# Optimization experiments

Hardware: AMD Instinct MI355X
Metric: run time of the kernel (lower is better)

The kernel has to match this reference:

```python
import jax, jax.numpy as jnp
import numpy as np

MAX_DEG = 10
MIN_DEG = 0
N_FEAT = 128
NB_FILTER = 128
BATCH = 128
DEG_COUNT = 30000                      # atoms per degree bucket (static)
N_ATOMS = (MAX_DEG + 1) * DEG_COUNT    # 330000, atoms sorted by degree (deg0 first)
NB_AFFINE = 3 * MAX_DEG + (2 - MIN_DEG)  # 32
EPS = 1e-5


def setup_inputs() -> dict:
    key = jax.random.key(0)
    ks = jax.random.split(key, 16)
    atoms = jax.random.normal(ks[0], (N_ATOMS, N_FEAT), dtype=jnp.float32)
    membership = jax.random.randint(ks[1], (N_ATOMS,), 0, BATCH)
    # deg_slice[d] = [start, count] for degree d (atoms sorted by degree)
    deg_slice = jnp.stack([jnp.arange(MAX_DEG + 1) * DEG_COUNT,
                           jnp.full((MAX_DEG + 1,), DEG_COUNT)], axis=1)
    inp = {"atoms": atoms, "deg_slice": deg_slice, "membership": membership}
    for d in range(1, MAX_DEG + 1):
        inp[f"adj{d}"] = jax.random.randint(ks[1 + d], (DEG_COUNT, d), 0, N_ATOMS)
    glorot = (2.0 / (N_FEAT + NB_FILTER)) ** 0.5
    inp["W"] = jax.random.normal(ks[12], (NB_AFFINE, N_FEAT, NB_FILTER), dtype=jnp.float32) * glorot
    inp["b"] = jnp.zeros((NB_AFFINE, NB_FILTER), dtype=jnp.float32)
    inp["gamma"] = jnp.ones((NB_FILTER,), dtype=jnp.float32)
    inp["beta"] = jnp.zeros((NB_FILTER,), dtype=jnp.float32)
    return inp


def _self_slice(atoms, deg):
    return jax.lax.dynamic_slice_in_dim(atoms, deg * DEG_COUNT, DEG_COUNT, axis=0)


def _norm(x, gamma, beta):
    m = jnp.mean(x, axis=-1, keepdims=True)
    std = jnp.sqrt(jnp.var(x, axis=-1, keepdims=True) + EPS)
    return gamma * ((x - m) / (std + EPS)) + beta


def _forward(atoms, W, b, gamma, beta, membership, adjs):
    # W consumption order matches the TF iterator: for deg=1..max_deg -> (rel, self),
    # then deg0 self at index 2*MAX_DEG, then gather affines deg1..max_deg, deg0 last.
    rel_outs = [None] * (MAX_DEG + 1)
    gather_outs = [None] * (MAX_DEG + 1)
    for d in range(1, MAX_DEG + 1):
        neigh = jnp.sum(atoms[adjs[d - 1]], axis=1)          # (COUNT, F) gather+sum
        self_a = _self_slice(atoms, d)                        # (COUNT, F)
        i_rel, i_self = 2 * (d - 1), 2 * d - 1
        rel_outs[d] = (neigh @ W[i_rel] + b[i_rel]) + (self_a @ W[i_self] + b[i_self])
        i_g = 2 * MAX_DEG + d
        gather_outs[d] = self_a @ W[i_g] + b[i_g]
    self0 = _self_slice(atoms, 0)
    rel_outs[0] = self0 @ W[2 * MAX_DEG] + b[2 * MAX_DEG]
    gather_outs[0] = self0 @ W[NB_AFFINE - 1] + b[NB_AFFINE - 1]

    activated = jnp.concatenate(rel_outs, axis=0)             # (N_ATOMS, NB_FILTER)
    gathered = jnp.concatenate(gather_outs, axis=0)           # (N_ATOMS, NB_FILTER)
    # graph_gather: per-molecule sum (dynamic_partition + reduce_sum)
    atom_gather = jax.ops.segment_sum(gathered, membership, num_segments=BATCH)

    xn = _norm(activated, gamma, beta)                        # per-row "BN" as in source
    yn = _norm(atom_gather, gamma, beta)
    # gather_node: per-molecule max of normalized atom features
    g = jax.ops.segment_max(xn, membership, num_segments=BATCH)
    return xn, yn, g


def reference(atoms, deg_slice, membership, adj1, adj2, adj3, adj4, adj5,
              adj6, adj7, adj8, adj9, adj10, W, b, gamma, beta):
    adjs = (adj1, adj2, adj3, adj4, adj5, adj6, adj7, adj8, adj9, adj10)
    return _forward(atoms, W, b, gamma, beta, membership, adjs)
```

## Files before the change

### kernel.cpp

```cpp
#include <hip/hip_runtime.h>
#include <stdint.h>

#define MAX_DEG   10
#define DEG_COUNT 30000
#define N_ATOMS   330000
#define NF        128
#define BATCH     128
#define SORT_BLOCKS 256

typedef __attribute__((ext_vector_type(8))) short bf16x8;
typedef __attribute__((ext_vector_type(4))) float f32x4;

__device__ __forceinline__ float bf2f(unsigned short h) {
  union { unsigned u; float f; } v; v.u = ((unsigned)h) << 16; return v.f;
}
__device__ __forceinline__ unsigned short f2bf(float f) {
  union { float f; unsigned u; } v; v.f = f;
  unsigned u = v.u;
  unsigned r = (u + 0x7fffu + ((u >> 16) & 1u)) >> 16;
  return (unsigned short)r;
}

struct AdjPtrs { const int* p[10]; };

#define NEG_INF_BITS 0xFF800000

__global__ __launch_bounds__(256) void k_cast(const float4* __restrict__ src,
                                              ushort4* __restrict__ dst) {
  size_t i = (size_t)blockIdx.x * 256 + threadIdx.x;
  float4 v = src[i];
  ushort4 o;
  o.x = f2bf(v.x); o.y = f2bf(v.y); o.z = f2bf(v.z); o.w = f2bf(v.w);
  dst[i] = o;
}

__global__ __launch_bounds__(256) void k_build_b(const float* __restrict__ W,
                                                 unsigned short* __restrict__ BcatT) {
  int idx = blockIdx.x * 256 + threadIdx.x;
  if (idx >= 11 * 256 * 256) return;
  int d = idx >> 16;
  int rem = idx & 65535;
  int n = rem >> 8;
  int k = rem & 255;
  float v = 0.f;
  if (k < 128) {
    if (n < 128 && d >= 1) v = W[(2 * (d - 1)) * 16384 + k * 128 + n];
  } else {
    int ks = k - 128;
    if (n < 128) { int wi = (d >= 1) ? (2 * d - 1) : 20; v = W[wi * 16384 + ks * 128 + n]; }
    else         { int wi = (d >= 1) ? (20 + d)   : 31; v = W[wi * 16384 + ks * 128 + (n - 128)]; }
  }
  BcatT[idx] = f2bf(v);
}

__global__ __launch_bounds__(256) void k_build_bias(const float* __restrict__ b,
                                                    float* __restrict__ biascat) {
  int idx = blockIdx.x * 256 + threadIdx.x;
  if (idx >= 11 * 256) return;
  int d = idx >> 8, n = idx & 255;
  float f;
  if (n < 128) {
    if (d >= 1) f = b[(2 * (d - 1)) * 128 + n] + b[(2 * d - 1) * 128 + n];
    else        f = b[20 * 128 + n];
  } else {
    int j = n - 128;
    f = (d >= 1) ? b[(20 + d) * 128 + j] : b[31 * 128 + j];
  }
  biascat[idx] = f;
}

template<int D>
__device__ __forceinline__ void nsum_phase0(const unsigned* __restrict__ atomsU,
                                            const int* __restrict__ abase,
                                            unsigned* __restrict__ NS,
                                            int rowTile, int wave, int lane) {
  for (int it = 0; it < 16; ++it) {
    int iloc = wave * 32 + it * 2;
    int r0 = rowTile * 256 + iloc;
    int sw0 = lane ^ ((iloc & 7) << 2);
    int sw1 = lane ^ (((iloc + 1) & 7) << 2);
    if (r0 < DEG_COUNT - 1) {
      const int* a = abase + (size_t)r0 * D;
      int myIdx = (lane < 2 * D) ? a[lane] : 0;
      unsigned xs[2 * D];
#pragma unroll
      for (int j = 0; j < 2 * D; ++j) {
        int nbr = __shfl(myIdx, j, 64);
        xs[j] = atomsU[(size_t)nbr * 64 + lane];
      }
      float s0a = 0.f, s1a = 0.f, s0b = 0.f, s1b = 0.f;
#pragma unroll
      for (int j = 0; j < D; ++j) {
        s0a += bf2f((unsigned short)(xs[j] & 0xffff));
        s1a += bf2f((unsigned short)(xs[j] >> 16));
      }
#pragma unroll
      for (int j = D; j < 2 * D; ++j) {
        s0b += bf2f((unsigned short)(xs[j] & 0xffff));
        s1b += bf2f((unsigned short)(xs[j] >> 16));
      }
      NS[(size_t)iloc * 64 + sw0]       = (unsigned)f2bf(s0a) | ((unsigned)f2bf(s1a) << 16);
      NS[(size_t)(iloc + 1) * 64 + sw1] = (unsigned)f2bf(s0b) | ((unsigned)f2bf(s1b) << 16);
    } else {
      const int* a = abase + (size_t)(DEG_COUNT - 1) * D;
      int myIdx = (lane < D) ? a[lane] : 0;
      unsigned xs[D];
#pragma unroll
      for (int j = 0; j < D; ++j) {
        int nbr = __shfl(myIdx, j, 64);
        xs[j] = atomsU[(size_t)nbr * 64 + lane];
      }
      float s0 = 0.f, s1 = 0.f;
#pragma unroll
      for (int j = 0; j < D; ++j) {
        s0 += bf2f((unsigned short)(xs[j] & 0xffff));
        s1 += bf2f((unsigned short)(xs[j] >> 16));
      }
      unsigned p = (unsigned)f2bf(s0) | ((unsigned)f2bf(s1) << 16);
      NS[(size_t)iloc * 64 + sw0] = p;
      NS[(size_t)(iloc + 1) * 64 + sw1] = p;
    }
  }
}

__global__ __launch_bounds__(512, 2) void k_gemm(
    const unsigned short* __restrict__ atomsBf,
    AdjPtrs adj,
    const unsigned short* __restrict__ BcatT,
    const float* __restrict__ biascat,
    const float* __restrict__ gamma,
    const float* __restrict__ beta,
    float* __restrict__ out0,
    unsigned short* __restrict__ gath)
{
  const int d = blockIdx.y;
  const int rowTile = blockIdx.x;
  const int tid = threadIdx.x;
  const int lane = tid & 63;
  const int wave = tid >> 6;
  const int m16 = lane & 15;
  const int g = lane >> 4;

  __shared__ unsigned short Bs[256 * 256];
  unsigned* NS = (unsigned*)Bs;

  const unsigned short* Bd = BcatT + d * 65536;
  const unsigned* atomsU = (const unsigned*)atomsBf;

  const int rowBase0 = rowTile * 256 + wave * 32;
  bf16x8 af0[8], af1[8];
  {
    int rbL = rowBase0 + m16; if (rbL > DEG_COUNT - 1) rbL = DEG_COUNT - 1;
    size_t gr = (size_t)d * DEG_COUNT + rbL;
#pragma unroll
    for (int ks = 4; ks < 8; ++ks)
      af0[ks] = *(const bf16x8*)(atomsBf + gr * 128 + (ks - 4) * 32 + g * 8);
  }
  {
    int rbL = rowBase0 + 16 + m16; if (rbL > DEG_COUNT - 1) rbL = DEG_COUNT - 1;
    size_t gr = (size_t)d * DEG_COUNT + rbL;
#pragma unroll
    for (int ks = 4; ks < 8; ++ks)
      af1[ks] = *(const bf16x8*)(atomsBf + gr * 128 + (ks - 4) * 32 + g * 8);
  }

  if (d > 0) {
    const int* abase = adj.p[d - 1];
    switch (d) {
      case 1:  nsum_phase0<1>(atomsU, abase, NS, rowTile, wave, lane); break;
      case 2:  nsum_phase0<2>(atomsU, abase, NS, rowTile, wave, lane); break;
      case 3:  nsum_phase0<3>(atomsU, abase, NS, rowTile, wave, lane); break;
      case 4:  nsum_phase0<4>(atomsU, abase, NS, rowTile, wave, lane); break;
      case 5:  nsum_phase0<5>(atomsU, abase, NS, rowTile, wave, lane); break;
      case 6:  nsum_phase0<6>(atomsU, abase, NS, rowTile, wave, lane); break;
      case 7:  nsum_phase0<7>(atomsU, abase, NS, rowTile, wave, lane); break;
      case 8:  nsum_phase0<8>(atomsU, abase, NS, rowTile, wave, lane); break;
      case 9:  nsum_phase0<9>(atomsU, abase, NS, rowTile, wave, lane); break;
      default: nsum_phase0<10>(atomsU, abase, NS, rowTile, wave, lane); break;
    }
    __syncthreads();
    const char* nsb = (const char*)NS;
    const int rowb0 = (wave * 32 + m16) * 256;
    const int rowb1 = (wave * 32 + 16 + m16) * 256;
    const int sw = (m16 & 7) << 4;
#pragma unroll
    for (int ks = 0; ks < 4; ++ks) {
      af0[ks] = *(const bf16x8*)(nsb + ((rowb0 + ks * 64 + g * 16) ^ sw));
      af1[ks] = *(const bf16x8*)(nsb + ((rowb1 + ks * 64 + g * 16) ^ sw));
    }
    __syncthreads();
  } else {
    bf16x8 z = {0, 0, 0, 0, 0, 0, 0, 0};
#pragma unroll
    for (int ks = 0; ks < 4; ++ks) { af0[ks] = z; af1[ks] = z; }
  }

#pragma unroll
  for (int it = 0; it < 16; ++it) {
    int flat = it * 512 + tid;
    int row = flat >> 5;
    int c = flat & 31;
    uint4 v = *(const uint4*)(Bd + row * 256 + c * 8);
    int kb = (c * 16) ^ ((row & 7) << 4);
    *(uint4*)((char*)Bs + row * 512 + kb) = v;
  }

  __syncthreads();

  const int ldsMask = (m16 & 7) << 4;

  f32x4 acc0[16], acc1[16];
#pragma unroll
  for (int ct = 0; ct < 16; ++ct) {
    acc0[ct] = (f32x4){0.f, 0.f, 0.f, 0.f};
    acc1[ct] = (f32x4){0.f, 0.f, 0.f, 0.f};
  }

#pragma unroll
  for (int ct = 0; ct < 16; ++ct) {
    const char* bbase = (const char*)Bs + (ct * 16 + m16) * 512;
    bf16x8 bf[8];
#pragma unroll
    for (int ks = 0; ks < 8; ++ks)
      bf[ks] = *(const bf16x8*)(bbase + ((ks * 64 + g * 16) ^ ldsMask));
#pragma unroll
    for (int ks = 0; ks < 8; ++ks) {
      acc0[ct] = __builtin_amdgcn_mfma_f32_16x16x32_bf16(af0[ks], bf[ks], acc0[ct], 0, 0, 0);
      acc1[ct] = __builtin_amdgcn_mfma_f32_16x16x32_bf16(af1[ks], bf[ks], acc1[ct], 0, 0, 0);
    }
  }

  float bias_[16], gam[8], bet[8];
#pragma unroll
  for (int ct = 0; ct < 16; ++ct) bias_[ct] = biascat[d * 256 + ct * 16 + m16];
#pragma unroll
  for (int ct = 0; ct < 8; ++ct) {
    gam[ct] = gamma[ct * 16 + m16];
    bet[ct] = beta[ct * 16 + m16];
  }

#pragma unroll
  for (int sub = 0; sub < 2; ++sub) {
    const int rowBase = rowBase0 + sub * 16;
    f32x4* acc = (sub == 0) ? acc0 : acc1;

#pragma unroll
    for (int ct = 0; ct < 16; ++ct)
#pragma unroll
      for (int r = 0; r < 4; ++r) acc[ct][r] += bias_[ct];

    float s[4], qq[4];
#pragma unroll
    for (int r = 0; r < 4; ++r) {
      s[r] = 0.f; qq[r] = 0.f;
#pragma unroll
      for (int ct = 0; ct < 8; ++ct) {
        float v = acc[ct][r];
        s[r] += v; qq[r] += v * v;
      }
    }
#pragma unroll
    for (int off = 8; off >= 1; off >>= 1) {
#pragma unroll
      for (int r = 0; r < 4; ++r) {
        s[r]  += __shfl_xor(s[r],  off, 64);
        qq[r] += __shfl_xor(qq[r], off, 64);
      }
    }

#pragma unroll
    for (int r = 0; r < 4; ++r) {
      int rb = rowBase + g * 4 + r;
      float mean = s[r] * (1.0f / 128.0f);
      float var  = qq[r] * (1.0f / 128.0f) - mean * mean;
      float inv  = 1.0f / (sqrtf(var + 1e-5f) + 1e-5f);
      if (rb < DEG_COUNT) {
        size_t grow = (size_t)d * DEG_COUNT + rb;
#pragma unroll
        for (int ct = 0; ct < 8; ++ct)
          out0[grow * 128 + ct * 16 + m16] = gam[ct] * ((acc[ct][r] - mean) * inv) + bet[ct];
#pragma unroll
        for (int ct = 8; ct < 16; ++ct)
          gath[grow * 128 + (ct - 8) * 16 + m16] = f2bf(acc[ct][r]);
      }
    }
  }
}

__global__ __launch_bounds__(256) void k_hist2(const int* __restrict__ membership,
                                               int* __restrict__ blockHist) {
  __shared__ int bins[BATCH];
  int tid = threadIdx.x;
  if (tid < BATCH) bins[tid] = 0;
  __syncthreads();
  const int chunk = (N_ATOMS + SORT_BLOCKS - 1) / SORT_BLOCKS;
  int lo = blockIdx.x * chunk, hi = min(lo + chunk, N_ATOMS);
  for (int i = lo + tid; i < hi; i += 256)
    atomicAdd(&bins[membership[i]], 1);
  __syncthreads();
  if (tid < BATCH) blockHist[blockIdx.x * BATCH + tid] = bins[tid];
}

__global__ __launch_bounds__(128) void k_scan2(const int* __restrict__ blockHist,
                                               int* __restrict__ off,
                                               int* __restrict__ base,
                                               int* __restrict__ hist) {
  int m = threadIdx.x;
  int tot = 0;
  for (int b = 0; b < SORT_BLOCKS; ++b) tot += blockHist[b * BATCH + m];
  hist[m] = tot;
  __shared__ int t[BATCH];
  t[m] = tot;
  __syncthreads();
  int acc = 0;
  for (int i = 0; i < m; ++i) acc += t[i];
  base[m] = acc;
  int run = acc;
  for (int b = 0; b < SORT_BLOCKS; ++b) {
    off[b * BATCH + m] = run;
    run += blockHist[b * BATCH + m];
  }
}

__global__ __launch_bounds__(256) void k_scatter2(const int* __restrict__ membership,
                                                  const int* __restrict__ off,
                                                  int* __restrict__ perm) {
  __shared__ int bins[BATCH];
  int tid = threadIdx.x;
  if (tid < BATCH) bins[tid] = off[blockIdx.x * BATCH + tid];
  __syncthreads();
  const int chunk = (N_ATOMS + SORT_BLOCKS - 1) / SORT_BLOCKS;
  int lo = blockIdx.x * chunk, hi = min(lo + chunk, N_ATOMS);
  for (int i = lo + tid; i < hi; i += 256) {
    int m = membership[i];
    int pos = atomicAdd(&bins[m], 1);
    perm[pos] = i;
  }
}

__global__ __launch_bounds__(512) void k_reduce(
    const float2* __restrict__ xnV,
    const unsigned* __restrict__ gathU,
    const int* __restrict__ perm,
    const int* __restrict__ base,
    const int* __restrict__ hist,
    float2* __restrict__ psum4,
    float2* __restrict__ pmax4)
{
  const int m = blockIdx.x >> 2;
  const int s = blockIdx.x & 3;
  const int b0 = base[m], cnt = hist[m];
  const int lo = b0 + (cnt * s) / 4;
  const int hi = b0 + (cnt * (s + 1)) / 4;
  const int wave = threadIdx.x >> 6, lane = threadIdx.x & 63;

  const float NEG_INF = __int_as_float((int)NEG_INF_BITS);
  float mx0 = NEG_INF, mx1 = NEG_INF, s0 = 0.f, s1 = 0.f;

#pragma unroll 4
  for (int i = lo + wave; i < hi; i += 8) {
    int r = perm[i];
    float2 x = xnV[(size_t)r * 64 + lane];
    unsigned gg = gathU[(size_t)r * 64 + lane];
    mx0 = fmaxf(mx0, x.x);
    mx1 = fmaxf(mx1, x.y);
    s0 += bf2f((unsigned short)(gg & 0xffff));
    s1 += bf2f((unsigned short)(gg >> 16));
  }

  __shared__ float2 sumT[8][64];
  __shared__ float2 maxT[8][64];
  sumT[wave][lane] = make_float2(s0, s1);
  maxT[wave][lane] = make_float2(mx0, mx1);
  __syncthreads();

  if (threadIdx.x < 64) {
    int l = threadIdx.x;
    float2 ss = sumT[0][l];
    float2 mm = maxT[0][l];
#pragma unroll
    for (int w = 1; w < 8; ++w) {
      float2 a = sumT[w][l]; ss.x += a.x; ss.y += a.y;
      float2 b = maxT[w][l]; mm.x = fmaxf(mm.x, b.x); mm.y = fmaxf(mm.y, b.y);
    }
    psum4[(s * 128 + m) * 64 + l] = ss;
    pmax4[(s * 128 + m) * 64 + l] = mm;
  }
}

__global__ __launch_bounds__(128) void k_final(
    const float* __restrict__ psum4,
    const float* __restrict__ pmax4,
    const float* __restrict__ gamma,
    const float* __restrict__ beta,
    float* __restrict__ out1,
    float* __restrict__ out2)
{
  int m = blockIdx.x;
  int j = threadIdx.x;
  float s = 0.f, g = __int_as_float((int)NEG_INF_BITS);
#pragma unroll
  for (int sl = 0; sl < 4; ++sl) {
    s += psum4[(sl * 128 + m) * 128 + j];
    g = fmaxf(g, pmax4[(sl * 128 + m) * 128 + j]);
  }
  out2[m * 128 + j] = g;

  float ws_ = s, wq = s * s;
#pragma unroll
  for (int off = 32; off >= 1; off >>= 1) {
    ws_ += __shfl_xor(ws_, off, 64);
    wq  += __shfl_xor(wq, off, 64);
  }
  __shared__ float red[4];
  int wave = j >> 6, lane = j & 63;
  if (lane == 0) { red[wave * 2] = ws_; red[wave * 2 + 1] = wq; }
  __syncthreads();
  float S = red[0] + red[2], Q = red[1] + red[3];
  float mean = S * (1.f / 128.f);
  float var = Q * (1.f / 128.f) - mean * mean;
  float inv = 1.f / (sqrtf(var + 1e-5f) + 1e-5f);
  float yn = gamma[j] * ((s - mean) * inv) + beta[j];
  out1[m * 128 + j] = yn;
}

extern "C" void kernel_launch(void* const* d_in, const int* in_sizes, int n_in,
                              void* d_out, int out_size, void* d_ws, size_t ws_size,
                              hipStream_t stream) {
  const float* atoms = (const float*)d_in[0];
  const int* membership = (const int*)d_in[2];
  AdjPtrs adj;
  for (int i = 0; i < 10; ++i) adj.p[i] = (const int*)d_in[3 + i];
  const float* W     = (const float*)d_in[13];
  const float* b     = (const float*)d_in[14];
  const float* gamma = (const float*)d_in[15];
  const float* beta  = (const float*)d_in[16];

  char* ws = (char*)d_ws;
  size_t off = 0;
  unsigned short* atomsBf = (unsigned short*)(ws + off); off += (size_t)N_ATOMS * 128 * 2;
  unsigned short* nsum    = (unsigned short*)(ws + off); off += (size_t)N_ATOMS * 128 * 2;
  unsigned short* gath    = (unsigned short*)(ws + off); off += (size_t)N_ATOMS * 128 * 2;
  unsigned short* BcatT   = (unsigned short*)(ws + off); off += (size_t)11 * 256 * 256 * 2;
  float* biascat          = (float*)(ws + off);          off += (size_t)11 * 256 * 4;
  (void)nsum;

  char* scr = (char*)atomsBf;
  int* perm      = (int*)(scr);
  int* hist      = (int*)(scr + 2 * 1024 * 1024);
  int* base_     = (int*)(scr + 2 * 1024 * 1024 + 1024);
  int* blockHist = (int*)(scr + 2 * 1024 * 1024 + 4096);
  int* offTab    = (int*)(scr + 2 * 1024 * 1024 + 4096 + SORT_BLOCKS * BATCH * 4);
  float* psum4   = (float*)(scr + 3 * 1024 * 1024);
  float* pmax4   = (float*)(scr + 3 * 1024 * 1024 + 256 * 1024);

  float* out0 = (float*)d_out;
  float* out1 = out0 + (size_t)N_ATOMS * 128;
  float* out2 = out1 + 16384;

  hipLaunchKernelGGL(k_cast, dim3(N_ATOMS * 128 / 4 / 256), dim3(256), 0, stream,
                     (const float4*)atoms, (ushort4*)atomsBf);
  hipLaunchKernelGGL(k_build_b, dim3((11 * 256 * 256 + 255) / 256), dim3(256), 0, stream, W, BcatT);
  hipLaunchKernelGGL(k_build_bias, dim3((11 * 256 + 255) / 256), dim3(256), 0, stream, b, biascat);
  hipLaunchKernelGGL(k_gemm, dim3(118, 11), dim3(512), 0, stream,
                     atomsBf, adj, BcatT, biascat, gamma, beta, out0, gath);
  hipLaunchKernelGGL(k_hist2, dim3(SORT_BLOCKS), dim3(256), 0, stream, membership, blockHist);
  hipLaunchKernelGGL(k_scan2, dim3(1), dim3(128), 0, stream, blockHist, offTab, base_, hist);
  hipLaunchKernelGGL(k_scatter2, dim3(SORT_BLOCKS), dim3(256), 0, stream, membership, offTab, perm);
  hipLaunchKernelGGL(k_reduce, dim3(512), dim3(512), 0, stream,
                     (const float2*)out0, (const unsigned*)gath, perm, base_, hist,
                     (float2*)psum4, (float2*)pmax4);
  hipLaunchKernelGGL(k_final, dim3(128), dim3(128), 0, stream,
                     psum4, pmax4, gamma, beta, out1, out2);
}
```

Before: 554.2 us.

## Reassociate graph gather: sum atoms per molecule and degree before projecting

The gather-affine projection is linear, so the per-molecule sum of projected atoms is replaced by summing raw bf16 atoms per (molecule, degree) bucket and then applying the gather weights once per molecule in a small kernel, with biases scaled by bucket counts. This drops half the GEMM output columns and the bf16 gath intermediate write and read. The GEMM tile shrinks to 128 rows and 128 output columns with a higher occupancy hint. It adds a new reduction pass over atoms and changes the rounding order of the gather output.

New measurement: 554.5 us. Within noise of the previous version (+0.1%).

```diff
diff --git a/kernel.cpp b/kernel.cpp
--- a/kernel.cpp
+++ b/kernel.cpp
@@ -37,18 +37,18 @@
 __global__ __launch_bounds__(256) void k_build_b(const float* __restrict__ W,
                                                  unsigned short* __restrict__ BcatT) {
   int idx = blockIdx.x * 256 + threadIdx.x;
-  if (idx >= 11 * 256 * 256) return;
-  int d = idx >> 16;
-  int rem = idx & 65535;
+  if (idx >= 11 * 128 * 256) return;
+  int d = idx >> 15;
+  int rem = idx & 32767;
   int n = rem >> 8;
   int k = rem & 255;
-  float v = 0.f;
+  float v;
   if (k < 128) {
-    if (n < 128 && d >= 1) v = W[(2 * (d - 1)) * 16384 + k * 128 + n];
+    v = (d >= 1) ? W[(2 * (d - 1)) * 16384 + k * 128 + n] : 0.f;
   } else {
     int ks = k - 128;
-    if (n < 128) { int wi = (d >= 1) ? (2 * d - 1) : 20; v = W[wi * 16384 + ks * 128 + n]; }
-    else         { int wi = (d >= 1) ? (20 + d)   : 31; v = W[wi * 16384 + ks * 128 + (n - 128)]; }
+    int wi = (d >= 1) ? (2 * d - 1) : 20;
+    v = W[wi * 16384 + ks * 128 + n];
   }
   BcatT[idx] = f2bf(v);
 }
@@ -56,16 +56,10 @@
 __global__ __launch_bounds__(256) void k_build_bias(const float* __restrict__ b,
                                                     float* __restrict__ biascat) {
   int idx = blockIdx.x * 256 + threadIdx.x;
-  if (idx >= 11 * 256) return;
-  int d = idx >> 8, n = idx & 255;
-  float f;
-  if (n < 128) {
-    if (d >= 1) f = b[(2 * (d - 1)) * 128 + n] + b[(2 * d - 1) * 128 + n];
-    else        f = b[20 * 128 + n];
-  } else {
-    int j = n - 128;
-    f = (d >= 1) ? b[(20 + d) * 128 + j] : b[31 * 128 + j];
-  }
+  if (idx >= 11 * 128) return;
+  int d = idx >> 7, n = idx & 127;
+  float f = (d >= 1) ? (b[(2 * (d - 1)) * 128 + n] + b[(2 * d - 1) * 128 + n])
+                     : b[20 * 128 + n];
   biascat[idx] = f;
 }
 
@@ -74,9 +68,9 @@
                                             const int* __restrict__ abase,
                                             unsigned* __restrict__ NS,
                                             int rowTile, int wave, int lane) {
-  for (int it = 0; it < 16; ++it) {
-    int iloc = wave * 32 + it * 2;
-    int r0 = rowTile * 256 + iloc;
+  for (int it = 0; it < 8; ++it) {
+    int iloc = wave * 16 + it * 2;
+    int r0 = rowTile * 128 + iloc;
     int sw0 = lane ^ ((iloc & 7) << 2);
     int sw1 = lane ^ (((iloc + 1) & 7) << 2);
     if (r0 < DEG_COUNT - 1) {
@@ -123,15 +117,14 @@
   }
 }
 
-__global__ __launch_bounds__(512, 2) void k_gemm(
+__global__ __launch_bounds__(512, 4) void k_gemm(
     const unsigned short* __restrict__ atomsBf,
     AdjPtrs adj,
     const unsigned short* __restrict__ BcatT,
     const float* __restrict__ biascat,
     const float* __restrict__ gamma,
     const float* __restrict__ beta,
-    float* __restrict__ out0,
-    unsigned short* __restrict__ gath)
+    float* __restrict__ out0)
 {
   const int d = blockIdx.y;
   const int rowTile = blockIdx.x;
@@ -141,27 +134,20 @@
   const int m16 = lane & 15;
   const int g = lane >> 4;
 
-  __shared__ unsigned short Bs[256 * 256];
+  __shared__ unsigned short Bs[128 * 256];
   unsigned* NS = (unsigned*)Bs;
 
-  const unsigned short* Bd = BcatT + d * 65536;
+  const unsigned short* Bd = BcatT + d * 32768;
   const unsigned* atomsU = (const unsigned*)atomsBf;
 
-  const int rowBase0 = rowTile * 256 + wave * 32;
-  bf16x8 af0[8], af1[8];
+  const int rowBase = rowTile * 128 + wave * 16;
+  bf16x8 af[8];
   {
-    int rbL = rowBase0 + m16; if (rbL > DEG_COUNT - 1) rbL = DEG_COUNT - 1;
+    int rbL = rowBase + m16; if (rbL > DEG_COUNT - 1) rbL = DEG_COUNT - 1;
     size_t gr = (size_t)d * DEG_COUNT + rbL;
 #pragma unroll
     for (int ks = 4; ks < 8; ++ks)
-      af0[ks] = *(const bf16x8*)(atomsBf + gr * 128 + (ks - 4) * 32 + g * 8);
-  }
-  {
-    int rbL = rowBase0 + 16 + m16; if (rbL > DEG_COUNT - 1) rbL = DEG_COUNT - 1;
-    size_t gr = (size_t)d * DEG_COUNT + rbL;
-#pragma unroll
-    for (int ks = 4; ks < 8; ++ks)
-      af1[ks] = *(const bf16x8*)(atomsBf + gr * 128 + (ks - 4) * 32 + g * 8);
+      af[ks] = *(const bf16x8*)(atomsBf + gr * 128 + (ks - 4) * 32 + g * 8);
   }
 
   if (d > 0) {
@@ -180,23 +166,20 @@
     }
     __syncthreads();
     const char* nsb = (const char*)NS;
-    const int rowb0 = (wave * 32 + m16) * 256;
-    const int rowb1 = (wave * 32 + 16 + m16) * 256;
+    const int rowb = (wave * 16 + m16) * 256;
     const int sw = (m16 & 7) << 4;
 #pragma unroll
-    for (int ks = 0; ks < 4; ++ks) {
-      af0[ks] = *(const bf16x8*)(nsb + ((rowb0 + ks * 64 + g * 16) ^ sw));
-      af1[ks] = *(const bf16x8*)(nsb + ((rowb1 + ks * 64 + g * 16) ^ sw));
-    }
+    for (int ks = 0; ks < 4; ++ks)
+      af[ks] = *(const bf16x8*)(nsb + ((rowb + ks * 64 + g * 16) ^ sw));
     __syncthreads();
   } else {
     bf16x8 z = {0, 0, 0, 0, 0, 0, 0, 0};
 #pragma unroll
-    for (int ks = 0; ks < 4; ++ks) { af0[ks] = z; af1[ks] = z; }
-  }
-
-#pragma unroll
-  for (int it = 0; it < 16; ++it) {
+    for (int ks = 0; ks < 4; ++ks) af[ks] = z;
+  }
+
+#pragma unroll
+  for (int it = 0; it < 8; ++it) {
     int flat = it * 512 + tid;
     int row = flat >> 5;
     int c = flat & 31;
@@ -209,80 +192,65 @@
 
   const int ldsMask = (m16 & 7) << 4;
 
-  f32x4 acc0[16], acc1[16];
-#pragma unroll
-  for (int ct = 0; ct < 16; ++ct) {
-    acc0[ct] = (f32x4){0.f, 0.f, 0.f, 0.f};
-    acc1[ct] = (f32x4){0.f, 0.f, 0.f, 0.f};
-  }
-
-#pragma unroll
-  for (int ct = 0; ct < 16; ++ct) {
+  f32x4 acc[8];
+#pragma unroll
+  for (int ct = 0; ct < 8; ++ct) acc[ct] = (f32x4){0.f, 0.f, 0.f, 0.f};
+
+#pragma unroll
+  for (int ct = 0; ct < 8; ++ct) {
     const char* bbase = (const char*)Bs + (ct * 16 + m16) * 512;
     bf16x8 bf[8];
 #pragma unroll
     for (int ks = 0; ks < 8; ++ks)
       bf[ks] = *(const bf16x8*)(bbase + ((ks * 64 + g * 16) ^ ldsMask));
 #pragma unroll
-    for (int ks = 0; ks < 8; ++ks) {
-      acc0[ct] = __builtin_amdgcn_mfma_f32_16x16x32_bf16(af0[ks], bf[ks], acc0[ct], 0, 0, 0);
-      acc1[ct] = __builtin_amdgcn_mfma_f32_16x16x32_bf16(af1[ks], bf[ks], acc1[ct], 0, 0, 0);
-    }
-  }
-
-  float bias_[16], gam[8], bet[8];
-#pragma unroll
-  for (int ct = 0; ct < 16; ++ct) bias_[ct] = biascat[d * 256 + ct * 16 + m16];
+    for (int ks = 0; ks < 8; ++ks)
+      acc[ct] = __builtin_amdgcn_mfma_f32_16x16x32_bf16(af[ks], bf[ks], acc[ct], 0, 0, 0);
+  }
+
+  float bias_[8], gam[8], bet[8];
 #pragma unroll
   for (int ct = 0; ct < 8; ++ct) {
+    bias_[ct] = biascat[d * 128 + ct * 16 + m16];
     gam[ct] = gamma[ct * 16 + m16];
     bet[ct] = beta[ct * 16 + m16];
   }
 
 #pragma unroll
-  for (int sub = 0; sub < 2; ++sub) {
-    const int rowBase = rowBase0 + sub * 16;
-    f32x4* acc = (sub == 0) ? acc0 : acc1;
-
-#pragma unroll
-    for (int ct = 0; ct < 16; ++ct)
-#pragma unroll
-      for (int r = 0; r < 4; ++r) acc[ct][r] += bias_[ct];
-
-    float s[4], qq[4];
+  for (int ct = 0; ct < 8; ++ct)
+#pragma unroll
+    for (int r = 0; r < 4; ++r) acc[ct][r] += bias_[ct];
+
+  float s[4], qq[4];
+#pragma unroll
+  for (int r = 0; r < 4; ++r) {
+    s[r] = 0.f; qq[r] = 0.f;
+#pragma unroll
+    for (int ct = 0; ct < 8; ++ct) {
+      float v = acc[ct][r];
+      s[r] += v; qq[r] += v * v;
+    }
+  }
+#pragma unroll
+  for (int off = 8; off >= 1; off >>= 1) {
 #pragma unroll
     for (int r = 0; r < 4; ++r) {
-      s[r] = 0.f; qq[r] = 0.f;
-#pragma unroll
-      for (int ct = 0; ct < 8; ++ct) {
-        float v = acc[ct][r];
-        s[r] += v; qq[r] += v * v;
-      }
-    }
-#pragma unroll
-    for (int off = 8; off >= 1; off >>= 1) {
-#pragma unroll
-      for (int r = 0; r < 4; ++r) {
-        s[r]  += __shfl_xor(s[r],  off, 64);
-        qq[r] += __shfl_xor(qq[r], off, 64);
-      }
-    }
-
-#pragma unroll
-    for (int r = 0; r < 4; ++r) {
-      int rb = rowBase + g * 4 + r;
-      float mean = s[r] * (1.0f / 128.0f);
-      float var  = qq[r] * (1.0f / 128.0f) - mean * mean;
-      float inv  = 1.0f / (sqrtf(var + 1e-5f) + 1e-5f);
-      if (rb < DEG_COUNT) {
-        size_t grow = (size_t)d * DEG_COUNT + rb;
-#pragma unroll
-        for (int ct = 0; ct < 8; ++ct)
-          out0[grow * 128 + ct * 16 + m16] = gam[ct] * ((acc[ct][r] - mean) * inv) + bet[ct];
-#pragma unroll
-        for (int ct = 8; ct < 16; ++ct)
-          gath[grow * 128 + (ct - 8) * 16 + m16] = f2bf(acc[ct][r]);
-      }
+      s[r]  += __shfl_xor(s[r],  off, 64);
+      qq[r] += __shfl_xor(qq[r], off, 64);
+    }
+  }
+
+#pragma unroll
+  for (int r = 0; r < 4; ++r) {
+    int rb = rowBase + g * 4 + r;
+    float mean = s[r] * (1.0f / 128.0f);
+    float var  = qq[r] * (1.0f / 128.0f) - mean * mean;
+    float inv  = 1.0f / (sqrtf(var + 1e-5f) + 1e-5f);
+    if (rb < DEG_COUNT) {
+      size_t grow = (size_t)d * DEG_COUNT + rb;
+#pragma unroll
+      for (int ct = 0; ct < 8; ++ct)
+        out0[grow * 128 + ct * 16 + m16] = gam[ct] * ((acc[ct][r] - mean) * inv) + bet[ct];
     }
   }
 }
@@ -338,13 +306,119 @@
   }
 }
 
-__global__ __launch_bounds__(512) void k_reduce(
-    const float2* __restrict__ xnV,
-    const unsigned* __restrict__ gathU,
+__global__ __launch_bounds__(512) void k_msum(
+    const unsigned* __restrict__ atomsU,
     const int* __restrict__ perm,
     const int* __restrict__ base,
     const int* __restrict__ hist,
-    float2* __restrict__ psum4,
+    float* __restrict__ Spart,
+    int* __restrict__ cntPart)
+{
+  const int m = blockIdx.x >> 2;
+  const int s = blockIdx.x & 3;
+  const int b0 = base[m], cnt = hist[m];
+  const int lo = b0 + (cnt * s) / 4;
+  const int hi = b0 + (cnt * (s + 1)) / 4;
+  const int wave = threadIdx.x >> 6, lane = threadIdx.x & 63;
+
+  __shared__ float S[8][11][128];
+  __shared__ int C[8][11];
+  for (int e = lane; e < 11 * 128; e += 64) S[wave][e >> 7][e & 127] = 0.f;
+  if (lane < 11) C[wave][lane] = 0;
+  __syncthreads();
+
+  for (int i = lo + wave; i < hi; i += 8) {
+    int r = perm[i];
+    int d = r / DEG_COUNT;
+    unsigned x = atomsU[(size_t)r * 64 + lane];
+    S[wave][d][lane]      += bf2f((unsigned short)(x & 0xffff));
+    S[wave][d][64 + lane] += bf2f((unsigned short)(x >> 16));
+    if (lane == 0) C[wave][d]++;
+  }
+  __syncthreads();
+
+  for (int e = threadIdx.x; e < 11 * 128; e += 512) {
+    int d = e >> 7, p = e & 127;
+    float t = 0.f;
+#pragma unroll
+    for (int w = 0; w < 8; ++w) t += S[w][d][p];
+    int col = (p < 64) ? (2 * p) : (2 * (p - 64) + 1);
+    Spart[(((size_t)s * 128 + m) * 11 + d) * 128 + col] = t;
+  }
+  if (threadIdx.x < 11) {
+    int t = 0;
+#pragma unroll
+    for (int w = 0; w < 8; ++w) t += C[w][threadIdx.x];
+    cntPart[((size_t)s * 128 + m) * 11 + threadIdx.x] = t;
+  }
+}
+
+__global__ __launch_bounds__(128) void k_yn(
+    const float* __restrict__ Spart,
+    const int* __restrict__ cntPart,
+    const float* __restrict__ W,
+    const float* __restrict__ b,
+    const float* __restrict__ gamma,
+    const float* __restrict__ beta,
+    float* __restrict__ out1)
+{
+  int m = blockIdx.x;
+  int j = threadIdx.x;
+  __shared__ float Sm[11][128];
+  __shared__ float cw[11];
+  for (int e = j; e < 11 * 128; e += 128) {
+    int d = e >> 7, c = e & 127;
+    float t = 0.f;
+#pragma unroll
+    for (int sl = 0; sl < 4; ++sl)
+      t += Spart[(((size_t)sl * 128 + m) * 11 + d) * 128 + c];
+    Sm[d][c] = t;
+  }
+  if (j < 11) {
+    int t = 0;
+#pragma unroll
+    for (int sl = 0; sl < 4; ++sl) t += cntPart[((size_t)sl * 128 + m) * 11 + j];
+    cw[j] = (float)t;
+  }
+  __syncthreads();
+
+  float acc = 0.f;
+  for (int d = 0; d < 11; ++d) {
+    int wi = (d >= 1) ? (20 + d) : 31;
+    const float* Wd = W + wi * 16384;
+    float a0 = 0.f, a1 = 0.f, a2 = 0.f, a3 = 0.f;
+    for (int k = 0; k < 128; k += 4) {
+      a0 += Sm[d][k]     * Wd[k * 128 + j];
+      a1 += Sm[d][k + 1] * Wd[(k + 1) * 128 + j];
+      a2 += Sm[d][k + 2] * Wd[(k + 2) * 128 + j];
+      a3 += Sm[d][k + 3] * Wd[(k + 3) * 128 + j];
+    }
+    acc += (a0 + a1) + (a2 + a3);
+    acc += cw[d] * b[wi * 128 + j];
+  }
+
+  float ws_ = acc, wq = acc * acc;
+#pragma unroll
+  for (int off = 32; off >= 1; off >>= 1) {
+    ws_ += __shfl_xor(ws_, off, 64);
+    wq  += __shfl_xor(wq, off, 64);
+  }
+  __shared__ float red[4];
+  int wave = j >> 6, lane = j & 63;
+  if (lane == 0) { red[wave * 2] = ws_; red[wave * 2 + 1] = wq; }
+  __syncthreads();
+  float Ssum = red[0] + red[2], Q = red[1] + red[3];
+  float mean = Ssum * (1.f / 128.f);
+  float var = Q * (1.f / 128.f) - mean * mean;
+  float inv = 1.f / (sqrtf(var + 1e-5f) + 1e-5f);
+  out1[m * 128 + j] = gamma[j] * ((acc - mean) * inv) + beta[j];
+}
+
+__global__ __launch_bounds__(512) void k_reduce(
+    const float2* __restrict__ xnV,
+    const int* __restrict__ perm,
+    const int* __restrict__ base,
+    const int* __restrict__ hist,
     float2* __restrict__ pmax4)
 {
   const int m = blockIdx.x >> 2;
@@ -355,73 +429,42 @@
   const int wave = threadIdx.x >> 6, lane = threadIdx.x & 63;
 
   const float NEG_INF = __int_as_float((int)NEG_INF_BITS);
-  float mx0 = NEG_INF, mx1 = NEG_INF, s0 = 0.f, s1 = 0.f;
+  float mx0 = NEG_INF, mx1 = NEG_INF;
 
 #pragma unroll 4
   for (int i = lo + wave; i < hi; i += 8) {
     int r = perm[i];
     float2 x = xnV[(size_t)r * 64 + lane];
-    unsigned gg = gathU[(size_t)r * 64 + lane];
     mx0 = fmaxf(mx0, x.x);
     mx1 = fmaxf(mx1, x.y);
-    s0 += bf2f((unsigned short)(gg & 0xffff));
-    s1 += bf2f((unsigned short)(gg >> 16));
-  }
-
-  __shared__ float2 sumT[8][64];
+  }
+
   __shared__ float2 maxT[8][64];
-  sumT[wave][lane] = make_float2(s0, s1);
   maxT[wave][lane] = make_float2(mx0, mx1);
   __syncthreads();
 
   if (threadIdx.x < 64) {
     int l = threadIdx.x;
-    float2 ss = sumT[0][l];
     float2 mm = maxT[0][l];
 #pragma unroll
     for (int w = 1; w < 8; ++w) {
-      float2 a = sumT[w][l]; ss.x += a.x; ss.y += a.y;
       float2 b = maxT[w][l]; mm.x = fmaxf(mm.x, b.x); mm.y = fmaxf(mm.y, b.y);
     }
-    psum4[(s * 128 + m) * 64 + l] = ss;
     pmax4[(s * 128 + m) * 64 + l] = mm;
   }
 }
 
 __global__ __launch_bounds__(128) void k_final(
-    const float* __restrict__ psum4,
     const float* __restrict__ pmax4,
-    const float* __restrict__ gamma,
-    const float* __restrict__ beta,
-    float* __restrict__ out1,
     float* __restrict__ out2)
 {
   int m = blockIdx.x;
   int j = threadIdx.x;
-  float s = 0.f, g = __int_as_float((int)NEG_INF_BITS);
-#pragma unroll
-  for (int sl = 0; sl < 4; ++sl) {
-    s += psum4[(sl * 128 + m) * 128 + j];
+  float g = __int_as_float((int)NEG_INF_BITS);
+#pragma unroll
+  for (int sl = 0; sl < 4; ++sl)
     g = fmaxf(g, pmax4[(sl * 128 + m) * 128 + j]);
-  }
   out2[m * 128 + j] = g;
-
-  float ws_ = s, wq = s * s;
-#pragma unroll
-  for (int off = 32; off >= 1; off >>= 1) {
-    ws_ += __shfl_xor(ws_, off, 64);
-    wq  += __shfl_xor(wq, off, 64);
-  }
-  __shared__ float red[4];
-  int wave = j >> 6, lane = j & 63;
-  if (lane == 0) { red[wave * 2] = ws_; red[wave * 2 + 1] = wq; }
-  __syncthreads();
-  float S = red[0] + red[2], Q = red[1] + red[3];
-  float mean = S * (1.f / 128.f);
-  float var = Q * (1.f / 128.f) - mean * mean;
-  float inv = 1.f / (sqrtf(var + 1e-5f) + 1e-5f);
-  float yn = gamma[j] * ((s - mean) * inv) + beta[j];
-  out1[m * 128 + j] = yn;
 }
 
 extern "C" void kernel_launch(void* const* d_in, const int* in_sizes, int n_in,
@@ -439,20 +482,16 @@
   char* ws = (char*)d_ws;
   size_t off = 0;
   unsigned short* atomsBf = (unsigned short*)(ws + off); off += (size_t)N_ATOMS * 128 * 2;
-  unsigned short* nsum    = (unsigned short*)(ws + off); off += (size_t)N_ATOMS * 128 * 2;
-  unsigned short* gath    = (unsigned short*)(ws + off); off += (size_t)N_ATOMS * 128 * 2;
-  unsigned short* BcatT   = (unsigned short*)(ws + off); off += (size_t)11 * 256 * 256 * 2;
-  float* biascat          = (float*)(ws + off);          off += (size_t)11 * 256 * 4;
-  (void)nsum;
-
-  char* scr = (char*)atomsBf;
-  int* perm      = (int*)(scr);
-  int* hist      = (int*)(scr + 2 * 1024 * 1024);
-  int* base_     = (int*)(scr + 2 * 1024 * 1024 + 1024);
-  int* blockHist = (int*)(scr + 2 * 1024 * 1024 + 4096);
-  int* offTab    = (int*)(scr + 2 * 1024 * 1024 + 4096 + SORT_BLOCKS * BATCH * 4);
-  float* psum4   = (float*)(scr + 3 * 1024 * 1024);
-  float* pmax4   = (float*)(scr + 3 * 1024 * 1024 + 256 * 1024);
+  unsigned short* BcatT   = (unsigned short*)(ws + off); off += (size_t)11 * 128 * 256 * 2;
+  float* biascat          = (float*)(ws + off);          off += (size_t)11 * 128 * 4;
+  int* perm               = (int*)(ws + off);            off += (size_t)N_ATOMS * 4;
+  int* hist               = (int*)(ws + off);            off += 512;
+  int* base_              = (int*)(ws + off);            off += 512;
+  int* blockHist          = (int*)(ws + off);            off += (size_t)SORT_BLOCKS * BATCH * 4;
+  int* offTab             = (int*)(ws + off);            off += (size_t)SORT_BLOCKS * BATCH * 4;
+  float* Spart            = (float*)(ws + off);          off += (size_t)4 * 128 * 11 * 128 * 4;
+  int* cntPart            = (int*)(ws + off);            off += (size_t)4 * 128 * 11 * 4;
+  float* pmax4            = (float*)(ws + off);          off += (size_t)4 * 128 * 128 * 4;
 
   float* out0 = (float*)d_out;
   float* out1 = out0 + (size_t)N_ATOMS * 128;
@@ -460,16 +499,18 @@
 
   hipLaunchKernelGGL(k_cast, dim3(N_ATOMS * 128 / 4 / 256), dim3(256), 0, stream,
                      (const float4*)atoms, (ushort4*)atomsBf);
-  hipLaunchKernelGGL(k_build_b, dim3((11 * 256 * 256 + 255) / 256), dim3(256), 0, stream, W, BcatT);
-  hipLaunchKernelGGL(k_build_bias, dim3((11 * 256 + 255) / 256), dim3(256), 0, stream, b, biascat);
-  hipLaunchKernelGGL(k_gemm, dim3(118, 11), dim3(512), 0, stream,
-                     atomsBf, adj, BcatT, biascat, gamma, beta, out0, gath);
+  hipLaunchKernelGGL(k_build_b, dim3((11 * 128 * 256 + 255) / 256), dim3(256), 0, stream, W, BcatT);
+  hipLaunchKernelGGL(k_build_bias, dim3((11 * 128 + 255) / 256), dim3(256), 0, stream, b, biascat);
   hipLaunchKernelGGL(k_hist2, dim3(SORT_BLOCKS), dim3(256), 0, stream, membership, blockHist);
   hipLaunchKernelGGL(k_scan2, dim3(1), dim3(128), 0, stream, blockHist, offTab, base_, hist);
   hipLaunchKernelGGL(k_scatter2, dim3(SORT_BLOCKS), dim3(256), 0, stream, membership, offTab, perm);
+  hipLaunchKernelGGL(k_msum, dim3(512), dim3(512), 0, stream,
+                     (const unsigned*)atomsBf, perm, base_, hist, Spart, cntPart);
+  hipLaunchKernelGGL(k_gemm, dim3(236, 11), dim3(512), 0, stream,
+                     atomsBf, adj, BcatT, biascat, gamma, beta, out0);
   hipLaunchKernelGGL(k_reduce, dim3(512), dim3(512), 0, stream,
-                     (const float2*)out0, (const unsigned*)gath, perm, base_, hist,
-                     (float2*)psum4, (float2*)pmax4);
-  hipLaunchKernelGGL(k_final, dim3(128), dim3(128), 0, stream,
-                     psum4, pmax4, gamma, beta, out1, out2);
-}
+                     (const float2*)out0, perm, base_, hist, (float2*)pmax4);
+  hipLaunchKernelGGL(k_yn, dim3(128), dim3(128), 0, stream,
+                     Spart, cntPart, W, b, gamma, beta, out1);
+  hipLaunchKernelGGL(k_final, dim3(128), dim3(128), 0, stream, pmax4, out2);
+}
```
